# Optimization experiments

Hardware: AMD Instinct MI355X
Metric: run time of the kernel (lower is better)

Reference implementation:

```python
import jax, jax.numpy as jnp
import numpy as np

B, S, D, MD = 4, 4096, 1024, 512
SCALE = 0.02  # init scale for weights


def _layernorm(x, g, b, eps=1e-5):
    m = jnp.mean(x, axis=-1, keepdims=True)
    v = jnp.mean((x - m) ** 2, axis=-1, keepdims=True)
    return (x - m) * jax.lax.rsqrt(v + eps) * g + b


def _mem_mlp(h, W0, W1):
    # MemoryMLP depth=2: linear -> gelu -> linear (no biases)
    return jax.nn.gelu(h @ W0) @ W1


def _assoc_scan(gates, inputs):
    # state_t = g_t * state_{t-1} + in_t, over the seq axis (axis=1)
    def step(state, gi):
        g, i = gi
        s = g * state + i
        return s, s
    init = jnp.zeros_like(inputs[:, 0])
    _, out = jax.lax.scan(step, init, (jnp.moveaxis(gates, 1, 0), jnp.moveaxis(inputs, 1, 0)))
    return jnp.moveaxis(out, 1, 0)


def setup_inputs() -> dict:
    key = jax.random.key(0)
    ks = jax.random.split(key, 10)
    return {
        "x": jax.random.normal(ks[0], (B, S, D), jnp.float32),
        "Wd": jax.random.normal(ks[1], (D, MD), jnp.float32) * SCALE,
        "bd": jnp.zeros((MD,), jnp.float32),
        "Wu": jax.random.normal(ks[2], (MD, D), jnp.float32) * SCALE,
        "bu": jnp.zeros((D,), jnp.float32),
        "Wq": jax.random.normal(ks[3], (MD, MD), jnp.float32) * SCALE,
        "bq": jnp.zeros((MD,), jnp.float32),
        "Wk": jax.random.normal(ks[4], (MD, MD), jnp.float32) * SCALE,
        "bk": jnp.zeros((MD,), jnp.float32),
        "Wv": jax.random.normal(ks[5], (MD, MD), jnp.float32) * SCALE,
        "bv": jnp.zeros((MD,), jnp.float32),
        "q_gamma": jnp.ones((MD,), jnp.float32),
        "q_beta": jnp.zeros((MD,), jnp.float32),
        "k_gamma": jnp.ones((MD,), jnp.float32),
        "k_beta": jnp.zeros((MD,), jnp.float32),
        "W0": jax.random.normal(ks[6], (MD, MD), jnp.float32) * SCALE,
        "W1": jax.random.normal(ks[7], (MD, MD), jnp.float32) * SCALE,
        "adaptive_lr": jnp.full((1,), 0.01, jnp.float32),
        "forget_factor": jnp.full((1,), 0.1, jnp.float32),
    }


def reference(x, Wd, bd, Wu, bu, Wq, bq, Wk, bk, Wv, bv,
              q_gamma, q_beta, k_gamma, k_beta, W0, W1,
              adaptive_lr, forget_factor):
    h = x @ Wd + bd                                   # [B,S,MD] down_proj
    q = _layernorm(h @ Wq + bq, q_gamma, q_beta)      # q_norm(to_queries)
    k = _layernorm(h @ Wk + bk, k_gamma, k_beta)      # k_norm(to_keys)
    v = h @ Wv + bv                                   # to_values
    retrieved = _mem_mlp(q, W0, W1)                   # memory read
    pred = _mem_mlp(k, W0, W1)                        # memory store pred
    # per-token surprise: MSE over feature dim
    surprise = jnp.mean((pred - v) ** 2, axis=-1, keepdims=True)  # [B,S,1]
    gate_val = 1.0 - jax.nn.sigmoid(forget_factor)[0]
    gates = jnp.full((B, S, 1), 1.0, jnp.float32) * gate_val
    inputs = adaptive_lr[0] * surprise * v            # surprise-weighted write
    scanned = _assoc_scan(gates, inputs)              # sequential recurrence
    out = (retrieved + scanned) @ Wu + bu             # up_proj
    return out
```

## Files before the change

### kernel.cpp

```cpp
#include <hip/hip_runtime.h>
#include <hip/hip_bf16.h>
#include <math.h>

#define B_    4
#define S_    4096
#define DD    1024
#define MD    512
#define NTOK  16384
#define CHUNK 32
#define NCH   128

typedef unsigned short u16;
typedef unsigned int u32;
typedef __attribute__((ext_vector_type(8))) short short8;
typedef __attribute__((ext_vector_type(4))) float f32x4;
typedef __attribute__((ext_vector_type(4))) unsigned short us4;

__device__ __forceinline__ float bf2f(u16 u) {
    u32 x = ((u32)u) << 16;
    return __builtin_bit_cast(float, x);
}
__device__ __forceinline__ u16 f2bf(float f) {
    u32 x = __builtin_bit_cast(u32, f);
    u32 lsb = (x >> 16) & 1u;
    x += 0x7fffu + lsb;
    return (u16)(x >> 16);
}
__device__ __forceinline__ float gelu_f(float x) {
    float x3 = x * x * x;
    return 0.5f * x * (1.0f + tanhf(0.7978845608028654f * (x + 0.044715f * x3)));
}
__device__ __forceinline__ float gate_from_ff(const float* ff) {
    return 1.0f - 1.0f / (1.0f + expf(-ff[0]));
}

#define GLDS(gp, lp) __builtin_amdgcn_global_load_lds( \
    (const __attribute__((address_space(1))) void*)(gp), \
    (__attribute__((address_space(3))) void*)(lp), 16, 0, 0)

template<int EPI, int HB, int OUTBF, int SEG>
__global__ __launch_bounds__(256) void gemm_bf16_k(
    const u16* __restrict__ A, const u16* __restrict__ BT,
    const float* __restrict__ bias0, const float* __restrict__ bias1,
    const float* __restrict__ bias2,
    void* __restrict__ out0, void* __restrict__ out1, void* __restrict__ out2,
    int K, int gx, int OM)
{
    __shared__ __align__(16) u16 Al[2][128 * 32];
    __shared__ __align__(16) u16 Bl[2][128 * 32];
    const int tid = threadIdx.x;
    const int w = tid >> 6, l = tid & 63;

    const int nwg = gridDim.x;
    const int cpx = nwg >> 3;
    const int o = blockIdx.x;
    const int swz = (o & 7) * cpx + (o >> 3);
    const int bx = swz % gx, by = swz / gx;

    const int rowBase = by * 128, colBase = bx * 128;
    const int wm = (w >> 1) * 64, wn = (w & 1) * 64;

    const int srow = l >> 2;
    const int skoff = (l & 3) * 8;
    const u16* Ag0 = A + (size_t)(rowBase + w * 16 + srow) * K + skoff;
    const u16* Ag1 = A + (size_t)(rowBase + (w + 4) * 16 + srow) * K + skoff;
    const u16* Bg0 = BT + (size_t)(colBase + w * 16 + srow) * K + skoff;
    const u16* Bg1 = BT + (size_t)(colBase + (w + 4) * 16 + srow) * K + skoff;

    f32x4 acc[4][4];
#pragma unroll
    for (int i = 0; i < 4; ++i)
#pragma unroll
        for (int j = 0; j < 4; ++j) acc[i][j] = (f32x4){0.f, 0.f, 0.f, 0.f};

    const int KT = K >> 5;
    GLDS(Ag0, &Al[0][(w * 16) * 32]);
    GLDS(Ag1, &Al[0][((w + 4) * 16) * 32]);
    GLDS(Bg0, &Bl[0][(w * 16) * 32]);
    GLDS(Bg1, &Bl[0][((w + 4) * 16) * 32]);
    __syncthreads();

    const int lr = l & 15;
    const int goff = (l >> 4) * 8;
    int cur = 0;
    for (int kt = 0; kt < KT; ++kt) {
        if (kt + 1 < KT) {
            const size_t ko = (size_t)(kt + 1) << 5;
            GLDS(Ag0 + ko, &Al[cur ^ 1][(w * 16) * 32]);
            GLDS(Ag1 + ko, &Al[cur ^ 1][((w + 4) * 16) * 32]);
            GLDS(Bg0 + ko, &Bl[cur ^ 1][(w * 16) * 32]);
            GLDS(Bg1 + ko, &Bl[cur ^ 1][((w + 4) * 16) * 32]);
        }
        short8 af[4], bfr[4];
#pragma unroll
        for (int m = 0; m < 4; ++m)
            af[m] = *(const short8*)&Al[cur][(wm + m * 16 + lr) * 32 + goff];
#pragma unroll
        for (int n = 0; n < 4; ++n)
            bfr[n] = *(const short8*)&Bl[cur][(wn + n * 16 + lr) * 32 + goff];
#pragma unroll
        for (int m = 0; m < 4; ++m)
#pragma unroll
            for (int n = 0; n < 4; ++n)
                acc[m][n] = __builtin_amdgcn_mfma_f32_16x16x32_bf16(af[m], bfr[n], acc[m][n], 0, 0, 0);
        __syncthreads();
        cur ^= 1;
    }

    const int g4 = (l >> 4) * 4;
    const int wcol0 = colBase + wn;
    const int seg = SEG ? (wcol0 >> 9) : 0;
    const int lcol0 = SEG ? (wcol0 - (seg << 9)) : wcol0;
    const float* bp = (seg == 0) ? bias0 : (seg == 1) ? bias1 : bias2;
    void* outp = (seg == 0) ? out0 : (seg == 1) ? out1 : out2;

    if (OUTBF) {
        u16* scr = &Al[0][0] + w * 1024;
        u16* ob = (u16*)outp;
        const bool odd = l & 1;
        const int lrp = lr & ~1;
#pragma unroll
        for (int m = 0; m < 4; ++m) {
            const int baseRow = rowBase + wm + m * 16;
            float vq[4][4];
#pragma unroll
            for (int n = 0; n < 4; ++n) {
                const float bj = HB ? bp[lcol0 + n * 16 + lr] : 0.0f;
#pragma unroll
                for (int q = 0; q < 4; ++q) {
                    float vv = acc[m][n][q] + bj;
                    if (EPI == 1) vv = gelu_f(vv);
                    vq[n][q] = vv;
                }
            }
#pragma unroll
            for (int n = 0; n < 4; ++n) {
                float pv[4];
#pragma unroll
                for (int q = 0; q < 4; ++q) pv[q] = __shfl_xor(vq[n][q], 1);
                const int q0 = odd ? 2 : 0;
#pragma unroll
                for (int j = 0; j < 2; ++j) {
                    const int qq = q0 + j;
                    float lo = odd ? pv[qq] : vq[n][qq];
                    float hi = odd ? vq[n][qq] : pv[qq];
                    u32 word = (u32)f2bf(lo) | ((u32)f2bf(hi) << 16);
                    *(u32*)&scr[(g4 + qq) * 64 + n * 16 + lrp] = word;
                }
            }
            asm volatile("s_waitcnt lgkmcnt(0)" ::: "memory");
            __builtin_amdgcn_sched_barrier(0);
            short8 r0 = *(const short8*)&scr[(l >> 3) * 64 + (l & 7) * 8];
            short8 r1 = *(const short8*)&scr[((l >> 3) + 8) * 64 + (l & 7) * 8];
            const size_t gaddr = (size_t)(baseRow + (l >> 3)) * OM + lcol0 + (l & 7) * 8;
            *(short8*)(ob + gaddr) = r0;
            *(short8*)(ob + gaddr + (size_t)8 * OM) = r1;
            __builtin_amdgcn_sched_barrier(0);
        }
    } else {
#pragma unroll
        for (int n = 0; n < 4; ++n) {
            const int col = lcol0 + n * 16 + lr;
            const float bj = HB ? bp[col] : 0.0f;
#pragma unroll
            for (int m = 0; m < 4; ++m) {
                const int row0 = rowBase + wm + m * 16 + g4;
#pragma unroll
                for (int q = 0; q < 4; ++q) {
                    float vv = acc[m][n][q] + bj;
                    if (EPI == 1) vv = gelu_f(vv);
                    ((float*)outp)[(size_t)(row0 + q) * OM + col] = vv;
                }
            }
        }
    }
}

__global__ __launch_bounds__(256) void cvt_bf16_k(const float* __restrict__ in,
                                                  u16* __restrict__ out, int n)
{
    size_t i = ((size_t)blockIdx.x * 256 + threadIdx.x) * 8;
    if (i + 8 > (size_t)n) return;
    float4 a = *(const float4*)(in + i);
    float4 b = *(const float4*)(in + i + 4);
    short8 o;
    o[0] = (short)f2bf(a.x); o[1] = (short)f2bf(a.y);
    o[2] = (short)f2bf(a.z); o[3] = (short)f2bf(a.w);
    o[4] = (short)f2bf(b.x); o[5] = (short)f2bf(b.y);
    o[6] = (short)f2bf(b.z); o[7] = (short)f2bf(b.w);
    *(short8*)(out + i) = o;
}

__global__ __launch_bounds__(256) void wtrans_k(const float* __restrict__ W,
                                                u16* __restrict__ WT, int K, int M)
{
    __shared__ float t[32][33];
    const int tx = threadIdx.x, ty = threadIdx.y;
    const int m0 = blockIdx.x * 32, k0 = blockIdx.y * 32;
#pragma unroll
    for (int i = 0; i < 4; ++i)
        t[ty + i * 8][tx] = W[(size_t)(k0 + ty + i * 8) * M + m0 + tx];
    __syncthreads();
#pragma unroll
    for (int i = 0; i < 4; ++i)
        WT[(size_t)(m0 + ty + i * 8) * K + k0 + tx] = f2bf(t[tx][ty + i * 8]);
}

__global__ __launch_bounds__(256) void wtrans5_k(
    const float* __restrict__ Wa, const float* __restrict__ Wb,
    const float* __restrict__ Wc, const float* __restrict__ Wd_,
    const float* __restrict__ We,
    u16* __restrict__ Ta, u16* __restrict__ Tb, u16* __restrict__ Tc,
    u16* __restrict__ Td, u16* __restrict__ Te)
{
    __shared__ float t[32][33];
    const float* W; u16* T;
    switch (blockIdx.z) {
        case 0: W = Wa; T = Ta; break;
        case 1: W = Wb; T = Tb; break;
        case 2: W = Wc; T = Tc; break;
        case 3: W = Wd_; T = Td; break;
        default: W = We; T = Te; break;
    }
    const int tx = threadIdx.x, ty = threadIdx.y;
    const int m0 = blockIdx.x * 32, k0 = blockIdx.y * 32;
#pragma unroll
    for (int i = 0; i < 4; ++i)
        t[ty + i * 8][tx] = W[(size_t)(k0 + ty + i * 8) * 512 + m0 + tx];
    __syncthreads();
#pragma unroll
    for (int i = 0; i < 4; ++i)
        T[(size_t)(m0 + ty + i * 8) * 512 + k0 + tx] = f2bf(t[tx][ty + i * 8]);
}

__global__ __launch_bounds__(256) void ln2_k(u16* __restrict__ X0, u16* __restrict__ X1,
                                             const float* __restrict__ g0, const float* __restrict__ b0,
                                             const float* __restrict__ g1, const float* __restrict__ b1)
{
    const int row = blockIdx.x, tid = threadIdx.x;
    u16* x = (blockIdx.y ? X1 : X0) + (size_t)row * MD;
    const float* g = blockIdx.y ? g1 : g0;
    const float* b = blockIdx.y ? b1 : b0;
    float v0 = bf2f(x[tid]), v1 = bf2f(x[tid + 256]);
    float s = v0 + v1, q = v0 * v0 + v1 * v1;
#pragma unroll
    for (int off = 32; off > 0; off >>= 1) {
        s += __shfl_down(s, off);
        q += __shfl_down(q, off);
    }
    __shared__ float redS[4], redQ[4];
    __shared__ float s_mean, s_rstd;
    const int lane = tid & 63, w = tid >> 6;
    if (lane == 0) { redS[w] = s; redQ[w] = q; }
    __syncthreads();
    if (tid == 0) {
        float S = redS[0] + redS[1] + redS[2] + redS[3];
        float Q = redQ[0] + redQ[1] + redQ[2] + redQ[3];
        float m = S * (1.f / 512.f);
        float var = Q * (1.f / 512.f) - m * m;
        s_mean = m; s_rstd = rsqrtf(var + 1e-5f);
    }
    __syncthreads();
    const float m = s_mean, rs = s_rstd;
    x[tid]       = f2bf((v0 - m) * rs * g[tid]       + b[tid]);
    x[tid + 256] = f2bf((v1 - m) * rs * g[tid + 256] + b[tid + 256]);
}

__global__ __launch_bounds__(256) void surprise_k(const u16* __restrict__ pred,
                                                  const u16* __restrict__ v,
                                                  const float* __restrict__ lr_p,
                                                  float* __restrict__ coef)
{
    const int row = blockIdx.x, tid = threadIdx.x;
    const u16* pp = pred + (size_t)row * MD;
    const u16* vp = v + (size_t)row * MD;
    float d0 = bf2f(pp[tid]) - bf2f(vp[tid]);
    float d1 = bf2f(pp[tid + 256]) - bf2f(vp[tid + 256]);
    float q = d0 * d0 + d1 * d1;
#pragma unroll
    for (int off = 32; off > 0; off >>= 1) q += __shfl_down(q, off);
    __shared__ float redQ[4];
    const int lane = tid & 63, w = tid >> 6;
    if (lane == 0) redQ[w] = q;
    __syncthreads();
    if (tid == 0) {
        float Q = redQ[0] + redQ[1] + redQ[2] + redQ[3];
        coef[row] = lr_p[0] * (Q * (1.f / 512.f));
    }
}

__global__ __launch_bounds__(256) void scan1_k(u16* __restrict__ io,
                                               const float* __restrict__ coef,
                                               const float* __restrict__ ff,
                                               float* __restrict__ carry)
{
    const int idx = blockIdx.x * blockDim.x + threadIdx.x;
    const int d4 = (idx & 127) * 4;
    const int c = (idx >> 7) & (NCH - 1);
    const int b = idx >> 14;
    const float g = gate_from_ff(ff);
    const int tok0 = b * S_ + c * CHUNK;
    u16* p = io + (size_t)tok0 * MD + d4;
    const float* cf = coef + tok0;
    float s0 = 0.f, s1 = 0.f, s2 = 0.f, s3 = 0.f;
#pragma unroll 4
    for (int t = 0; t < CHUNK; ++t) {
        us4 vv = *(const us4*)(p + (size_t)t * MD);
        const float ct = cf[t];
        s0 = fmaf(g, s0, ct * bf2f(vv.x));
        s1 = fmaf(g, s1, ct * bf2f(vv.y));
        s2 = fmaf(g, s2, ct * bf2f(vv.z));
        s3 = fmaf(g, s3, ct * bf2f(vv.w));
        us4 ov = { f2bf(s0), f2bf(s1), f2bf(s2), f2bf(s3) };
        *(us4*)(p + (size_t)t * MD) = ov;
    }
    float4 cw = { s0, s1, s2, s3 };
    *(float4*)(carry + ((size_t)b * NCH + c) * MD + d4) = cw;
}

__global__ __launch_bounds__(256) void scan2_k(const float* __restrict__ carry,
                                               const float* __restrict__ ff,
                                               float* __restrict__ Sin)
{
    const int idx = blockIdx.x * blockDim.x + threadIdx.x;
    const int d = idx & (MD - 1);
    const int b = idx >> 9;
    const float g = gate_from_ff(ff);
    const float gL = powf(g, (float)CHUNK);
    float p = 0.f;
    for (int c = 0; c < NCH; ++c) {
        Sin[((size_t)b * NCH + c) * MD + d] = p;
        p = carry[((size_t)b * NCH + c) * MD + d] + gL * p;
    }
}

__global__ __launch_bounds__(256) void scan3_k(const u16* __restrict__ loc,
                                               const float* __restrict__ Sin,
                                               const u16* __restrict__ retr,
                                               const float* __restrict__ ff,
                                               u16* __restrict__ fin)
{
    const size_t idx = (size_t)blockIdx.x * blockDim.x + threadIdx.x;
    const int d4 = (int)(idx & 127) * 4;
    const int t = (int)((idx >> 7) & (S_ - 1));
    const int b = (int)(idx >> 19);
    const int c = t >> 5, tl = t & (CHUNK - 1);
    const float g = gate_from_ff(ff);
    const float f = exp2f((float)(tl + 1) * log2f(g));
    const size_t row = (size_t)(b * S_ + t) * MD + d4;
    us4 lv = *(const us4*)(loc + row);
    us4 rv = *(const us4*)(retr + row);
    float4 sv = *(const float4*)(Sin + ((size_t)b * NCH + c) * MD + d4);
    us4 ov;
    ov.x = f2bf(bf2f(lv.x) + f * sv.x + bf2f(rv.x));
    ov.y = f2bf(bf2f(lv.y) + f * sv.y + bf2f(rv.y));
    ov.z = f2bf(bf2f(lv.z) + f * sv.z + bf2f(rv.z));
    ov.w = f2bf(bf2f(lv.w) + f * sv.w + bf2f(rv.w));
    *(us4*)(fin + row) = ov;
}

extern "C" void kernel_launch(void* const* d_in, const int* in_sizes, int n_in,
                              void* d_out, int out_size, void* d_ws, size_t ws_size,
                              hipStream_t stream) {
    const float* x   = (const float*)d_in[0];
    const float* Wd  = (const float*)d_in[1];
    const float* bd  = (const float*)d_in[2];
    const float* Wu  = (const float*)d_in[3];
    const float* bu  = (const float*)d_in[4];
    const float* Wq  = (const float*)d_in[5];
    const float* bq  = (const float*)d_in[6];
    const float* Wk  = (const float*)d_in[7];
    const float* bk  = (const float*)d_in[8];
    const float* Wv  = (const float*)d_in[9];
    const float* bv  = (const float*)d_in[10];
    const float* qg  = (const float*)d_in[11];
    const float* qb  = (const float*)d_in[12];
    const float* kg  = (const float*)d_in[13];
    const float* kb  = (const float*)d_in[14];
    const float* W0  = (const float*)d_in[15];
    const float* W1  = (const float*)d_in[16];
    const float* lr  = (const float*)d_in[17];
    const float* ff  = (const float*)d_in[18];
    float* out = (float*)d_out;

    u16* wdT   = (u16*)d_ws;
    u16* wqkvT = wdT + 512 * 1024;
    u16* w0T   = wqkvT + 1536 * 512;
    u16* w1T   = w0T + 512 * 512;
    u16* wuT   = w1T + 512 * 512;
    u16* xb    = wuT + 1024 * 512;
    u16* hb    = xb + (size_t)NTOK * DD;
    u16* b1    = hb + (size_t)NTOK * MD;
    u16* b2    = b1 + (size_t)NTOK * MD;
    u16* VB    = b2 + (size_t)NTOK * MD;
    float* coef  = (float*)(VB + (size_t)NTOK * MD);
    float* carry = coef + NTOK;
    float* Sin   = carry + (size_t)B_ * NCH * MD;

    dim3 blk(256);
    dim3 t32(32, 8);

    cvt_bf16_k<<<(NTOK * DD) / (256 * 8), blk, 0, stream>>>(x, xb, NTOK * DD);
    wtrans_k<<<dim3(16, 32), t32, 0, stream>>>(Wd, wdT, 1024, 512);
    wtrans5_k<<<dim3(16, 16, 5), t32, 0, stream>>>(Wq, Wk, Wv, W0, W1,
        wqkvT, wqkvT + 512 * 512, wqkvT + 2 * 512 * 512, w0T, w1T);
    wtrans_k<<<dim3(32, 16), t32, 0, stream>>>(Wu, wuT, 512, 1024);

    gemm_bf16_k<0, 1, 1, 0><<<dim3(512), blk, 0, stream>>>(
        xb, wdT, bd, bd, bd, hb, hb, hb, 1024, 4, 512);
    gemm_bf16_k<0, 1, 1, 1><<<dim3(1536), blk, 0, stream>>>(
        hb, wqkvT, bq, bk, bv, b1, b2, VB, 512, 12, 512);
    ln2_k<<<dim3(NTOK, 2), blk, 0, stream>>>(b1, b2, qg, qb, kg, kb);
    gemm_bf16_k<1, 0, 1, 0><<<dim3(1024), blk, 0, stream>>>(
        b1, w0T, nullptr, nullptr, nullptr, xb, xb, xb, 512, 4, 512);
    gemm_bf16_k<0, 0, 1, 0><<<dim3(1024), blk, 0, stream>>>(
        xb, w1T, nullptr, nullptr, nullptr, b1, b1, b1, 512, 4, 512);
    surprise_k<<<NTOK, blk, 0, stream>>>(b2, VB, lr, coef);
    scan1_k<<<(B_ * NCH * (MD / 4)) / 256, blk, 0, stream>>>(VB, coef, ff, carry);
    scan2_k<<<(B_ * MD) / 256, blk, 0, stream>>>(carry, ff, Sin);
    scan3_k<<<(NTOK * (MD / 4)) / 256, blk, 0, stream>>>(VB, Sin, b1, ff, b2);
    gemm_bf16_k<0, 1, 0, 0><<<dim3(1024), blk, 0, stream>>>(
        b2, wuT, bu, bu, bu, out, out, out, 512, 8, 1024);
}
```

Baseline: 330.6 us.

## Double GEMM K-tile to 64 with XOR-swizzled LDS and split fused launches

The bf16 MFMA GEMM now stages 64-wide K tiles instead of 32. Each loop iteration runs two MFMA sub-steps, which halves the number of barriers and loop iterations. Rows are stored in LDS with an XOR swizzle on 16-byte chunks, meant to avoid bank conflicts on the fragment reads. The segmented multi-output path is removed, so the fused QKV GEMM and the stacked q/k memory-MLP GEMMs become separate launches, with an extra scratch buffer for the activations. In exchange, LDS per block doubles to 64KB, which may lower occupancy, and there are more kernel launches.

```diff
diff --git a/kernel.cpp b/kernel.cpp
--- a/kernel.cpp
+++ b/kernel.cpp
@@ -38,16 +38,18 @@
     (const __attribute__((address_space(1))) void*)(gp), \
     (__attribute__((address_space(3))) void*)(lp), 16, 0, 0)
 
-template<int EPI, int HB, int OUTBF, int SEG>
+__device__ __forceinline__ int swzoff(int row, int byteInRow) {
+    return ((row * 128 + byteInRow) ^ ((row & 7) << 4)) >> 1;
+}
+
+template<int EPI, int HB, int OUTBF>
 __global__ __launch_bounds__(256) void gemm_bf16_k(
     const u16* __restrict__ A, const u16* __restrict__ BT,
-    const float* __restrict__ bias0, const float* __restrict__ bias1,
-    const float* __restrict__ bias2,
-    void* __restrict__ out0, void* __restrict__ out1, void* __restrict__ out2,
+    const float* __restrict__ bias, void* __restrict__ outp,
     int K, int gx, int OM)
 {
-    __shared__ __align__(16) u16 Al[2][128 * 32];
-    __shared__ __align__(16) u16 Bl[2][128 * 32];
+    __shared__ __align__(16) u16 Al[2][128 * 64];
+    __shared__ __align__(16) u16 Bl[2][128 * 64];
     const int tid = threadIdx.x;
     const int w = tid >> 6, l = tid & 63;
 
@@ -60,12 +62,16 @@
     const int rowBase = by * 128, colBase = bx * 128;
     const int wm = (w >> 1) * 64, wn = (w & 1) * 64;
 
-    const int srow = l >> 2;
-    const int skoff = (l & 3) * 8;
-    const u16* Ag0 = A + (size_t)(rowBase + w * 16 + srow) * K + skoff;
-    const u16* Ag1 = A + (size_t)(rowBase + (w + 4) * 16 + srow) * K + skoff;
-    const u16* Bg0 = BT + (size_t)(colBase + w * 16 + srow) * K + skoff;
-    const u16* Bg1 = BT + (size_t)(colBase + (w + 4) * 16 + srow) * K + skoff;
+    const int srow = l >> 3;
+    const int skoff = ((l & 7) ^ (l >> 3)) * 8;
+    const u16* Ag[4];
+    const u16* Bg[4];
+#pragma unroll
+    for (int j = 0; j < 4; ++j) {
+        const int seg = w * 4 + j;
+        Ag[j] = A  + (size_t)(rowBase + seg * 8 + srow) * K + skoff;
+        Bg[j] = BT + (size_t)(colBase + seg * 8 + srow) * K + skoff;
+    }
 
     f32x4 acc[4][4];
 #pragma unroll
@@ -73,46 +79,47 @@
 #pragma unroll
         for (int j = 0; j < 4; ++j) acc[i][j] = (f32x4){0.f, 0.f, 0.f, 0.f};
 
-    const int KT = K >> 5;
-    GLDS(Ag0, &Al[0][(w * 16) * 32]);
-    GLDS(Ag1, &Al[0][((w + 4) * 16) * 32]);
-    GLDS(Bg0, &Bl[0][(w * 16) * 32]);
-    GLDS(Bg1, &Bl[0][((w + 4) * 16) * 32]);
+    const int KT = K >> 6;
+
+#define STAGE(kt, buf) do { \
+    const size_t ko = (size_t)(kt) << 6; \
+    _Pragma("unroll") \
+    for (int j = 0; j < 4; ++j) { \
+        GLDS(Ag[j] + ko, &Al[buf][(w * 4 + j) * 512]); \
+        GLDS(Bg[j] + ko, &Bl[buf][(w * 4 + j) * 512]); \
+    } \
+} while (0)
+
+    STAGE(0, 0);
     __syncthreads();
 
     const int lr = l & 15;
-    const int goff = (l >> 4) * 8;
+    const int gb = (l >> 4) * 16;
     int cur = 0;
     for (int kt = 0; kt < KT; ++kt) {
-        if (kt + 1 < KT) {
-            const size_t ko = (size_t)(kt + 1) << 5;
-            GLDS(Ag0 + ko, &Al[cur ^ 1][(w * 16) * 32]);
-            GLDS(Ag1 + ko, &Al[cur ^ 1][((w + 4) * 16) * 32]);
-            GLDS(Bg0 + ko, &Bl[cur ^ 1][(w * 16) * 32]);
-            GLDS(Bg1 + ko, &Bl[cur ^ 1][((w + 4) * 16) * 32]);
+        if (kt + 1 < KT) STAGE(kt + 1, cur ^ 1);
+#pragma unroll
+        for (int ks = 0; ks < 2; ++ks) {
+            short8 af[4], bfr[4];
+#pragma unroll
+            for (int m = 0; m < 4; ++m)
+                af[m] = *(const short8*)&Al[cur][swzoff(wm + m * 16 + lr, ks * 64 + gb)];
+#pragma unroll
+            for (int n = 0; n < 4; ++n)
+                bfr[n] = *(const short8*)&Bl[cur][swzoff(wn + n * 16 + lr, ks * 64 + gb)];
+#pragma unroll
+            for (int m = 0; m < 4; ++m)
+#pragma unroll
+                for (int n = 0; n < 4; ++n)
+                    acc[m][n] = __builtin_amdgcn_mfma_f32_16x16x32_bf16(af[m], bfr[n], acc[m][n], 0, 0, 0);
         }
-        short8 af[4], bfr[4];
-#pragma unroll
-        for (int m = 0; m < 4; ++m)
-            af[m] = *(const short8*)&Al[cur][(wm + m * 16 + lr) * 32 + goff];
-#pragma unroll
-        for (int n = 0; n < 4; ++n)
-            bfr[n] = *(const short8*)&Bl[cur][(wn + n * 16 + lr) * 32 + goff];
-#pragma unroll
-        for (int m = 0; m < 4; ++m)
-#pragma unroll
-            for (int n = 0; n < 4; ++n)
-                acc[m][n] = __builtin_amdgcn_mfma_f32_16x16x32_bf16(af[m], bfr[n], acc[m][n], 0, 0, 0);
         __syncthreads();
         cur ^= 1;
     }
+#undef STAGE
 
     const int g4 = (l >> 4) * 4;
-    const int wcol0 = colBase + wn;
-    const int seg = SEG ? (wcol0 >> 9) : 0;
-    const int lcol0 = SEG ? (wcol0 - (seg << 9)) : wcol0;
-    const float* bp = (seg == 0) ? bias0 : (seg == 1) ? bias1 : bias2;
-    void* outp = (seg == 0) ? out0 : (seg == 1) ? out1 : out2;
+    const int col0 = colBase + wn;
 
     if (OUTBF) {
         u16* scr = &Al[0][0] + w * 1024;
@@ -125,7 +132,7 @@
             float vq[4][4];
 #pragma unroll
             for (int n = 0; n < 4; ++n) {
-                const float bj = HB ? bp[lcol0 + n * 16 + lr] : 0.0f;
+                const float bj = HB ? bias[col0 + n * 16 + lr] : 0.0f;
 #pragma unroll
                 for (int q = 0; q < 4; ++q) {
                     float vv = acc[m][n][q] + bj;
@@ -152,7 +159,7 @@
             __builtin_amdgcn_sched_barrier(0);
             short8 r0 = *(const short8*)&scr[(l >> 3) * 64 + (l & 7) * 8];
             short8 r1 = *(const short8*)&scr[((l >> 3) + 8) * 64 + (l & 7) * 8];
-            const size_t gaddr = (size_t)(baseRow + (l >> 3)) * OM + lcol0 + (l & 7) * 8;
+            const size_t gaddr = (size_t)(baseRow + (l >> 3)) * OM + col0 + (l & 7) * 8;
             *(short8*)(ob + gaddr) = r0;
             *(short8*)(ob + gaddr + (size_t)8 * OM) = r1;
             __builtin_amdgcn_sched_barrier(0);
@@ -160,8 +167,8 @@
     } else {
 #pragma unroll
         for (int n = 0; n < 4; ++n) {
-            const int col = lcol0 + n * 16 + lr;
-            const float bj = HB ? bp[col] : 0.0f;
+            const int col = col0 + n * 16 + lr;
+            const float bj = HB ? bias[col] : 0.0f;
 #pragma unroll
             for (int m = 0; m < 4; ++m) {
                 const int row0 = rowBase + wm + m * 16 + g4;
@@ -384,8 +391,10 @@
     float* out = (float*)d_out;
 
     u16* wdT   = (u16*)d_ws;
-    u16* wqkvT = wdT + 512 * 1024;
-    u16* w0T   = wqkvT + 1536 * 512;
+    u16* wqT   = wdT + 512 * 1024;
+    u16* wkT   = wqT + 512 * 512;
+    u16* wvT   = wkT + 512 * 512;
+    u16* w0T   = wvT + 512 * 512;
     u16* w1T   = w0T + 512 * 512;
     u16* wuT   = w1T + 512 * 512;
     u16* xb    = wuT + 1024 * 512;
@@ -393,7 +402,8 @@
     u16* b1    = hb + (size_t)NTOK * MD;
     u16* b2    = b1 + (size_t)NTOK * MD;
     u16* VB    = b2 + (size_t)NTOK * MD;
-    float* coef  = (float*)(VB + (size_t)NTOK * MD);
+    u16* ax    = VB + (size_t)NTOK * MD;
+    float* coef  = (float*)(ax + (size_t)NTOK * MD);
     float* carry = coef + NTOK;
     float* Sin   = carry + (size_t)B_ * NCH * MD;
 
@@ -403,22 +413,21 @@
     cvt_bf16_k<<<(NTOK * DD) / (256 * 8), blk, 0, stream>>>(x, xb, NTOK * DD);
     wtrans_k<<<dim3(16, 32), t32, 0, stream>>>(Wd, wdT, 1024, 512);
     wtrans5_k<<<dim3(16, 16, 5), t32, 0, stream>>>(Wq, Wk, Wv, W0, W1,
-        wqkvT, wqkvT + 512 * 512, wqkvT + 2 * 512 * 512, w0T, w1T);
+        wqT, wkT, wvT, w0T, w1T);
     wtrans_k<<<dim3(32, 16), t32, 0, stream>>>(Wu, wuT, 512, 1024);
 
-    gemm_bf16_k<0, 1, 1, 0><<<dim3(512), blk, 0, stream>>>(
-        xb, wdT, bd, bd, bd, hb, hb, hb, 1024, 4, 512);
-    gemm_bf16_k<0, 1, 1, 1><<<dim3(1536), blk, 0, stream>>>(
-        hb, wqkvT, bq, bk, bv, b1, b2, VB, 512, 12, 512);
+    gemm_bf16_k<0, 1, 1><<<dim3(512), blk, 0, stream>>>(xb, wdT, bd, hb, 1024, 4, 512);
+    gemm_bf16_k<0, 1, 1><<<dim3(512), blk, 0, stream>>>(hb, wqT, bq, b1, 512, 4, 512);
+    gemm_bf16_k<0, 1, 1><<<dim3(512), blk, 0, stream>>>(hb, wkT, bk, b2, 512, 4, 512);
+    gemm_bf16_k<0, 1, 1><<<dim3(512), blk, 0, stream>>>(hb, wvT, bv, VB, 512, 4, 512);
     ln2_k<<<dim3(NTOK, 2), blk, 0, stream>>>(b1, b2, qg, qb, kg, kb);
-    gemm_bf16_k<1, 0, 1, 0><<<dim3(1024), blk, 0, stream>>>(
-        b1, w0T, nullptr, nullptr, nullptr, xb, xb, xb, 512, 4, 512);
-    gemm_bf16_k<0, 0, 1, 0><<<dim3(1024), blk, 0, stream>>>(
-        xb, w1T, nullptr, nullptr, nullptr, b1, b1, b1, 512, 4, 512);
+    gemm_bf16_k<1, 0, 1><<<dim3(512), blk, 0, stream>>>(b1, w0T, nullptr, ax, 512, 4, 512);
+    gemm_bf16_k<0, 0, 1><<<dim3(512), blk, 0, stream>>>(ax, w1T, nullptr, b1, 512, 4, 512);
+    gemm_bf16_k<1, 0, 1><<<dim3(512), blk, 0, stream>>>(b2, w0T, nullptr, ax, 512, 4, 512);
+    gemm_bf16_k<0, 0, 1><<<dim3(512), blk, 0, stream>>>(ax, w1T, nullptr, b2, 512, 4, 512);
     surprise_k<<<NTOK, blk, 0, stream>>>(b2, VB, lr, coef);
     scan1_k<<<(B_ * NCH * (MD / 4)) / 256, blk, 0, stream>>>(VB, coef, ff, carry);
     scan2_k<<<(B_ * MD) / 256, blk, 0, stream>>>(carry, ff, Sin);
-    scan3_k<<<(NTOK * (MD / 4)) / 256, blk, 0, stream>>>(VB, Sin, b1, ff, b2);
-    gemm_bf16_k<0, 1, 0, 0><<<dim3(1024), blk, 0, stream>>>(
-        b2, wuT, bu, bu, bu, out, out, out, 512, 8, 1024);
-}
+    scan3_k<<<(NTOK * (MD / 4)) / 256, blk, 0, stream>>>(VB, Sin, b1, ff, ax);
+    gemm_bf16_k<0, 1, 0><<<dim3(1024), blk, 0, stream>>>(ax, wuT, bu, out, 512, 8, 1024);
+}
```

After: 332.8 us. Within noise of the previous version (+0.7%).
